# Performance work log

Hardware: AMD Instinct MI355X
Metric: run time of the kernel (lower is better)

## Reference

```python
import jax, jax.numpy as jnp
import numpy as np
import math


def _favor(X, W, is_query):
    # X: [B,L,H,M], W: [M,M] (shared across batch, matching tf.repeat of a single QR matrix)
    M = X.shape[-1]
    dn = 1.0 / math.sqrt(math.sqrt(M))
    X = dn * X
    diag = (jnp.sum(X * X, axis=-1) * (0.5 * dn * dn))[..., None]  # [B,L,H,1]
    dot = jnp.einsum('dm,blhm->blhd', W, X)                         # [B,L,H,M]
    if is_query:
        mx = jnp.max(X, axis=-1, keepdims=True)
    else:
        mx = jnp.max(X, axis=(1, 3), keepdims=True)  # axes (-3,-1) = (L, M)
    return (1.0 / math.sqrt(M)) * jnp.exp(dot - diag - mx + 1e-8)


def _causal_attn(qs, ks, vs):
    # qs,ks: [B,L,H,M]; vs: [B,L,H,D]. Cumulative KV-state recurrence via lax.scan.
    B, L, H, M = ks.shape
    D = vs.shape[-1]

    def step(carry, x):
        sums, snorm = carry          # [B,H,M,D], [B,H,M]
        q, k, v = x                  # [B,H,M], [B,H,M], [B,H,D]
        snorm = snorm + k
        sums = sums + k[..., :, None] * v[..., None, :]
        num = jnp.einsum('bhmd,bhm->bhd', sums, q)
        den = jnp.sum(q * snorm, axis=-1, keepdims=True)
        return (sums, snorm), num / den

    init = (jnp.zeros((B, H, M, D), qs.dtype), jnp.zeros((B, H, M), qs.dtype))
    xs = (jnp.swapaxes(qs, 0, 1), jnp.swapaxes(ks, 0, 1), jnp.swapaxes(vs, 0, 1))
    _, out = jax.lax.scan(step, init, xs)   # out: [L,B,H,D]
    return jnp.swapaxes(out, 0, 1)          # [B,L,H,D]


def _make_favor_proj(rng, M):
    # Mirrors: W ~ N(0,1); Q,_ = qr(W); Q /= norm(Q, axis=-1) (TF broadcast divides columns); Q *= sqrt(M)
    W = rng.standard_normal((M, M)).astype(np.float32)
    Q, _ = np.linalg.qr(W)
    n = np.linalg.norm(Q, axis=1)          # row norms, shape (M,)
    Q = Q / n[None, :]                     # TF broadcasting quirk: divide column j by n[j]
    return jnp.asarray(Q * math.sqrt(M), dtype=jnp.float32)


def setup_inputs() -> dict:
    B, L, d_model, H = 2, 4096, 1024, 16
    M = d_model // H
    key = jax.random.key(0)
    k1, k2, k3 = jax.random.split(key, 3)
    rng = np.random.default_rng(0)

    def dense_w(dout):
        return jnp.asarray(rng.standard_normal((d_model, dout)).astype(np.float32) * 0.02)

    return {
        'queries': jax.random.normal(k1, (B, L, d_model), jnp.float32),
        'keys': jax.random.normal(k2, (B, L, d_model), jnp.float32),
        'values': jax.random.normal(k3, (B, L, d_model), jnp.float32),
        'Wq': dense_w(H * M), 'bq': jnp.zeros((H * M,), jnp.float32),
        'Wk': dense_w(H * M), 'bk': jnp.zeros((H * M,), jnp.float32),
        'Wv': dense_w(H * M), 'bv': jnp.zeros((H * M,), jnp.float32),
        'Wo': dense_w(d_model), 'bo': jnp.zeros((d_model,), jnp.float32),
        'Wfq': _make_favor_proj(rng, M),
        'Wfk': _make_favor_proj(rng, M),
        'H': H,
    }


def reference(queries, keys, values, Wq, bq, Wk, bk, Wv, bv, Wo, bo, Wfq, Wfk, H):
    N, L, _ = queries.shape
    S = keys.shape[1]
    q = (queries @ Wq + bq).reshape(N, L, H, -1)
    k = (keys @ Wk + bk).reshape(N, S, H, -1)
    v = (values @ Wv + bv).reshape(N, S, H, -1)
    Ql = _favor(q, Wfq, is_query=True)
    Kl = _favor(k, Wfk, is_query=False)
    V = _causal_attn(Ql, Kl, v)             # [N,L,H,D]
    return V.reshape(N, L, -1) @ Wo + bo    # [N,L,d_model]
```

## Files before the change

### kernel.cpp

```cpp
#include <hip/hip_runtime.h>
#include <math.h>

#define BATCH 2
#define SEQ   4096
#define DM    1024
#define NH    16
#define MD    64
#define NROW  (BATCH*SEQ)
#define RQ    (BATCH*SEQ*NH)
#define NCHUNK 64
#define CT     64
#define DN    0.35355339059327373f
#define INV_SQRT_M 0.125f
#define PITCH 72
#define STSZ  (65*64)
#define DIAG_SCALE (0.125f * 0.0625f)

typedef unsigned short ushort_t;
typedef short bf8_t __attribute__((ext_vector_type(8)));
typedef float f4_t  __attribute__((ext_vector_type(4)));
typedef ushort_t us8_t __attribute__((ext_vector_type(8)));

__device__ static inline ushort_t f2bf(float f) {
    union { float f; unsigned u; } v; v.f = f;
    unsigned r = v.u + 0x7FFFu + ((v.u >> 16) & 1u);
    return (ushort_t)(r >> 16);
}
__device__ static inline float bf2f(ushort_t u) {
    union { unsigned u; float f; } v; v.u = ((unsigned)u) << 16;
    return v.f;
}

__device__ static inline void async_ld16(const ushort_t* g, ushort_t* l) {
    __builtin_amdgcn_global_load_lds(
        (const __attribute__((address_space(1))) unsigned int*)g,
        (__attribute__((address_space(3))) unsigned int*)l,
        16, 0, 0);
}

__device__ static inline void sbar() {
    __builtin_amdgcn_sched_barrier(0);
    __builtin_amdgcn_s_barrier();
    __builtin_amdgcn_sched_barrier(0);
}
#define VMCNT(n) do { asm volatile("s_waitcnt vmcnt(" #n ")" ::: "memory"); \
                      __builtin_amdgcn_sched_barrier(0); } while (0)

__device__ static inline void swz256(int bx, int* bm, int* bn) {
    const int xcd = bx & 7, s = bx >> 3;
    *bm = (xcd * 8 + (s >> 2)) << 7;
    *bn = (s & 3) << 8;
}

#define ABUF (128*64)
#define BBUF (256*64)

__device__ static inline void gemm128_core(
    const ushort_t* __restrict__ A, const ushort_t* __restrict__ BT,
    ushort_t* As, ushort_t* Bs, int bm, int bn, int tid, f4_t acc[4][4])
{
    const int lane = tid & 63, w = tid >> 6;
    const int wr = w >> 2, wc = w & 3;
    const int quad = lane >> 4, l15 = lane & 15;
    const int lrow = lane >> 3;
    const int kcol = ((lane & 7) ^ lrow) * 8;

    auto stB = [&](int t, int s) {
        #pragma unroll
        for (int c = 0; c < 4; ++c) {
            const int r0 = c * 64 + w * 8;
            async_ld16(BT + (size_t)(bn + r0 + lrow) * DM + t * 64 + kcol,
                       &Bs[s * BBUF + r0 * 64]);
        }
    };
    auto stA1 = [&](int t, int s) {
        const int r0 = (w < 4) ? w * 8 : 32 + w * 8;
        async_ld16(A + (size_t)(bm + r0 + lrow) * DM + t * 64 + kcol,
                   &As[s * ABUF + r0 * 64]);
    };
    auto stA2 = [&](int t, int s) {
        const int r0 = (w < 4) ? 32 + w * 8 : 64 + w * 8;
        async_ld16(A + (size_t)(bm + r0 + lrow) * DM + t * 64 + kcol,
                   &As[s * ABUF + r0 * 64]);
    };

    auto loadB = [&](int s, bf8_t bf[2][4]) {
        #pragma unroll
        for (int ks = 0; ks < 2; ++ks) {
            const int slot8 = (((ks << 2) | quad) ^ (l15 & 7)) * 8;
            #pragma unroll
            for (int j = 0; j < 4; ++j) {
                const int row = wc * 64 + j * 16 + l15;
                bf[ks][j] = *(const bf8_t*)&Bs[s * BBUF + row * 64 + slot8];
            }
        }
    };
    auto loadA = [&](int s, int ih, bf8_t af[2][2]) {
        #pragma unroll
        for (int ks = 0; ks < 2; ++ks) {
            const int slot8 = (((ks << 2) | quad) ^ (l15 & 7)) * 8;
            #pragma unroll
            for (int i = 0; i < 2; ++i) {
                const int row = wr * 64 + (ih * 2 + i) * 16 + l15;
                af[ks][i] = *(const bf8_t*)&As[s * ABUF + row * 64 + slot8];
            }
        }
    };
    auto mfma16 = [&](int ih, bf8_t af[2][2], bf8_t bf[2][4]) {
        __builtin_amdgcn_s_setprio(1);
        #pragma unroll
        for (int ks = 0; ks < 2; ++ks)
            #pragma unroll
            for (int i = 0; i < 2; ++i)
                #pragma unroll
                for (int j = 0; j < 4; ++j)
                    acc[ih * 2 + i][j] = __builtin_amdgcn_mfma_f32_16x16x32_bf16(
                        af[ks][i], bf[ks][j], acc[ih * 2 + i][j], 0, 0, 0);
        __builtin_amdgcn_s_setprio(0);
    };

    stB(0, 0); stA1(0, 0);
    stA2(0, 0);
    stB(1, 1); stA1(1, 1);
    VMCNT(6);
    sbar();

    bf8_t bf[2][4], af[2][2];
    #pragma unroll 1
    for (int v = 0; v < 7; ++v) {
        const int u0 = 2 * v;
        loadB(0, bf); loadA(0, 0, af);
        stA2(u0 + 1, 1);
        VMCNT(6); sbar();
        mfma16(0, af, bf);
        sbar();
        loadA(0, 1, af);
        stB(u0 + 2, 0); stA1(u0 + 2, 0);
        VMCNT(6); sbar();
        mfma16(1, af, bf);
        sbar();
        loadB(1, bf); loadA(1, 0, af);
        stA2(u0 + 2, 0);
        VMCNT(6); sbar();
        mfma16(0, af, bf);
        sbar();
        loadA(1, 1, af);
        stB(u0 + 3, 1); stA1(u0 + 3, 1);
        VMCNT(6); sbar();
        mfma16(1, af, bf);
        sbar();
    }
    loadB(0, bf); loadA(0, 0, af);
    stA2(15, 1);
    VMCNT(6); sbar();
    mfma16(0, af, bf);
    sbar();
    loadA(0, 1, af);
    VMCNT(1); sbar();
    mfma16(1, af, bf);
    sbar();
    loadB(1, bf); loadA(1, 0, af);
    VMCNT(0); sbar();
    mfma16(0, af, bf);
    sbar();
    loadA(1, 1, af);
    mfma16(1, af, bf);
}

__global__ __launch_bounds__(256) void prep_weights(
    const float* __restrict__ W0, const float* __restrict__ W1,
    const float* __restrict__ W2, const float* __restrict__ W3,
    ushort_t* __restrict__ WT, unsigned* __restrict__ kmOrd)
{
    if (blockIdx.z == 0 && blockIdx.x == 0 && blockIdx.y == 0 && threadIdx.x < 32)
        kmOrd[threadIdx.x] = 0u;
    const float* W = blockIdx.z == 0 ? W0 : (blockIdx.z == 1 ? W1 : (blockIdx.z == 2 ? W2 : W3));
    ushort_t* dst = WT + (size_t)blockIdx.z * DM * DM;
    __shared__ float t[32][33];
    const int k0 = blockIdx.x * 32, n0 = blockIdx.y * 32;
    const int tx = threadIdx.x & 31, ty = threadIdx.x >> 5;
    #pragma unroll
    for (int r = 0; r < 32; r += 8)
        t[ty + r][tx] = W[(size_t)(k0 + ty + r) * 1024 + n0 + tx];
    __syncthreads();
    #pragma unroll
    for (int r = 0; r < 32; r += 8)
        dst[(size_t)(n0 + ty + r) * 1024 + k0 + tx] = f2bf(t[tx][ty + r]);
}

__global__ __launch_bounds__(256) void cvt_qkv(
    const float* __restrict__ Q, const float* __restrict__ K,
    const float* __restrict__ V, ushort_t* __restrict__ Y)
{
    const int y = blockIdx.y;
    const float* X = y == 0 ? Q : (y == 1 ? K : V);
    ushort_t* dst = Y + (size_t)y * NROW * DM;
    int i = blockIdx.x * 256 + threadIdx.x;
    const float4* X4 = (const float4*)X;
    float4 a = X4[i * 2], b = X4[i * 2 + 1];
    us8_t o;
    o[0]=f2bf(a.x); o[1]=f2bf(a.y); o[2]=f2bf(a.z); o[3]=f2bf(a.w);
    o[4]=f2bf(b.x); o[5]=f2bf(b.y); o[6]=f2bf(b.z); o[7]=f2bf(b.w);
    *(us8_t*)&dst[i * 8] = o;
}

__global__ __launch_bounds__(512, 2) void gemm_qkv(
    const ushort_t* __restrict__ Xc, const ushort_t* __restrict__ WT,
    const float* __restrict__ bq, const float* __restrict__ bk,
    const float* __restrict__ bv, ushort_t* __restrict__ Obase,
    unsigned* __restrict__ kmOrd)
{
    __shared__ ushort_t As[2 * ABUF];
    __shared__ ushort_t Bs[2 * BBUF];
    const int z = blockIdx.y;
    const ushort_t* A  = Xc + (size_t)z * NROW * DM;
    const ushort_t* BT = WT + (size_t)z * DM * DM;
    const float* bias = z == 0 ? bq : (z == 1 ? bk : bv);
    ushort_t* Cbf = Obase + (size_t)z * NROW * DM;

    const int tid = threadIdx.x;
    int bm, bn;
    swz256(blockIdx.x, &bm, &bn);
    const int lane = tid & 63, w = tid >> 6;
    const int wr = w >> 2, wc = w & 3;
    const int quad = lane >> 4, l15 = lane & 15;

    f4_t acc[4][4] = {};
    gemm128_core(A, BT, As, Bs, bm, bn, tid, acc);

    float mx = -3.4e38f;
    #pragma unroll
    for (int j = 0; j < 4; ++j) {
        const int col = bn + wc * 64 + j * 16 + l15;
        const float bb = bias[col];
        #pragma unroll
        for (int i = 0; i < 4; ++i) {
            const int row0 = bm + wr * 64 + i * 16 + quad * 4;
            #pragma unroll
            for (int r = 0; r < 4; ++r) {
                float v = acc[i][j][r] + bb;
                mx = fmaxf(mx, v);
                Cbf[(size_t)(row0 + r) * DM + col] = f2bf(v);
            }
        }
    }
    if (z == 1) {
        #pragma unroll
        for (int off = 32; off; off >>= 1) mx = fmaxf(mx, __shfl_xor(mx, off));
        if (lane == 0) {
            const int b = bm >> 12;
            const int h = (bn + wc * 64) >> 6;
            unsigned ub = __float_as_uint(mx);
            unsigned enc = (ub & 0x80000000u) ? ~ub : (ub | 0x80000000u);
            atomicMax(&kmOrd[b * NH + h], enc);
        }
    }
}

__global__ __launch_bounds__(512, 2) void gemm_out(
    const ushort_t* __restrict__ A, const ushort_t* __restrict__ BT,
    const float* __restrict__ bias, float* __restrict__ C)
{
    __shared__ ushort_t As[2 * ABUF];
    __shared__ ushort_t Bs[2 * BBUF];
    const int tid = threadIdx.x;
    int bm, bn;
    swz256(blockIdx.x, &bm, &bn);
    const int lane = tid & 63, w = tid >> 6;
    const int wr = w >> 2, wc = w & 3;
    const int quad = lane >> 4, l15 = lane & 15;

    f4_t acc[4][4] = {};
    gemm128_core(A, BT, As, Bs, bm, bn, tid, acc);

    #pragma unroll
    for (int j = 0; j < 4; ++j) {
        const int col = bn + wc * 64 + j * 16 + l15;
        const float bb = bias[col];
        #pragma unroll
        for (int i = 0; i < 4; ++i) {
            const int row0 = bm + wr * 64 + i * 16 + quad * 4;
            #pragma unroll
            for (int r = 0; r < 4; ++r)
                C[(size_t)(row0 + r) * DM + col] = acc[i][j][r] + bb;
        }
    }
}

__global__ __launch_bounds__(256) void chunk_sums_mfma(
    const ushort_t* __restrict__ Kbf, const ushort_t* __restrict__ Vbf,
    const float* __restrict__ Wfk, const unsigned* __restrict__ kmOrd,
    ushort_t* __restrict__ ST)
{
    const int bx = blockIdx.x;
    const int c = bx & 63, h = (bx >> 6) & 15, b = bx >> 10;
    __shared__ ushort_t Ks[64 * PITCH];
    __shared__ ushort_t Kt[64 * PITCH];
    __shared__ ushort_t Vt[80 * PITCH];
    __shared__ ushort_t Ws[64 * PITCH];
    __shared__ float ssp[64][4];
    __shared__ float diag[64];
    const int tid = threadIdx.x;
    const int lane = tid & 63, w = tid >> 6;
    const int quad = lane >> 4, l15 = lane & 15;

    const size_t gbase = ((size_t)(b * SEQ + c * CT)) * DM + h * MD;

    #pragma unroll
    for (int r = 0; r < 2; ++r) {
        int idx = tid + r * 256;
        int row = idx >> 3, ch = idx & 7;
        *(us8_t*)&Ks[row * PITCH + ch * 8] =
            *(const us8_t*)&Kbf[gbase + (size_t)row * DM + ch * 8];
    }
    #pragma unroll
    for (int r = 0; r < 2; ++r) {
        int ch = w + r * 4;
        int t = lane;
        us8_t vv = *(const us8_t*)&Vbf[gbase + (size_t)t * DM + ch * 8];
        #pragma unroll
        for (int j = 0; j < 8; ++j) Vt[(ch * 8 + j) * PITCH + t] = vv[j];
    }
    if (tid < 64) Vt[64 * PITCH + tid] = (ushort_t)0x3F80;
    const float4* Wf4 = (const float4*)Wfk;
    #pragma unroll
    for (int i = 0; i < 4; ++i) {
        int f4i = tid + i * 256;
        int row = f4i >> 4, q4 = f4i & 15;
        float4 wv = Wf4[f4i];
        Ws[row * PITCH + q4 * 4 + 0] = f2bf(DN * wv.x);
        Ws[row * PITCH + q4 * 4 + 1] = f2bf(DN * wv.y);
        Ws[row * PITCH + q4 * 4 + 2] = f2bf(DN * wv.z);
        Ws[row * PITCH + q4 * 4 + 3] = f2bf(DN * wv.w);
    }
    __syncthreads();

    {
        const int row = tid >> 2, seg = tid & 3;
        const us8_t* xp = (const us8_t*)&Ks[row * PITCH + seg * 16];
        us8_t a = xp[0], b2 = xp[1];
        float ss = 0.f;
        #pragma unroll
        for (int j = 0; j < 8; ++j) {
            float x0 = bf2f(a[j]), x1 = bf2f(b2[j]);
            ss += x0 * x0 + x1 * x1;
        }
        ssp[row][seg] = ss;
    }
    __syncthreads();
    if (tid < 64)
        diag[tid] = (ssp[tid][0] + ssp[tid][1] + ssp[tid][2] + ssp[tid][3]) * DIAG_SCALE;
    unsigned u = kmOrd[b * NH + h];
    unsigned bits = (u & 0x80000000u) ? (u & 0x7FFFFFFFu) : ~u;
    const float mxs = DN * __uint_as_float(bits);
    __syncthreads();

    {
        bf8_t xf[2];
        #pragma unroll
        for (int ks = 0; ks < 2; ++ks)
            xf[ks] = *(const bf8_t*)&Ks[(w * 16 + l15) * PITCH + ks * 32 + quad * 8];
        f4_t facc[4] = {};
        #pragma unroll
        for (int dt = 0; dt < 4; ++dt)
            #pragma unroll
            for (int ks = 0; ks < 2; ++ks) {
                bf8_t wfr = *(const bf8_t*)&Ws[(dt * 16 + l15) * PITCH + ks * 32 + quad * 8];
                facc[dt] = __builtin_amdgcn_mfma_f32_16x16x32_bf16(xf[ks], wfr, facc[dt], 0, 0, 0);
            }
        #pragma unroll
        for (int r = 0; r < 4; ++r) {
            int t = w * 16 + quad * 4 + r;
            float d_ = diag[t];
            #pragma unroll
            for (int dt = 0; dt < 4; ++dt) {
                float e = facc[dt][r] - d_ - mxs + 1e-8f;
                Kt[(dt * 16 + l15) * PITCH + t] = f2bf(INV_SQRT_M * expf(e));
            }
        }
    }
    __syncthreads();

    ushort_t* Sg = ST + (size_t)((b * NH + h) * NCHUNK + c) * STSZ;

    bf8_t vf[2];
    #pragma unroll
    for (int ks = 0; ks < 2; ++ks)
        vf[ks] = *(const bf8_t*)&Vt[(w * 16 + l15) * PITCH + ks * 32 + quad * 8];
    f4_t acc[4] = {};
    #pragma unroll
    for (int mt = 0; mt < 4; ++mt)
        #pragma unroll
        for (int ks = 0; ks < 2; ++ks) {
            bf8_t kf = *(const bf8_t*)&Kt[(mt * 16 + l15) * PITCH + ks * 32 + quad * 8];
            acc[mt] = __builtin_amdgcn_mfma_f32_16x16x32_bf16(vf[ks], kf, acc[mt], 0, 0, 0);
        }
    #pragma unroll
    for (int mt = 0; mt < 4; ++mt)
        #pragma unroll
        for (int r = 0; r < 4; ++r)
            Sg[(w * 16 + quad * 4 + r) * 64 + mt * 16 + l15] = f2bf(acc[mt][r]);

    if (w == 0) {
        bf8_t vf4[2];
        #pragma unroll
        for (int ks = 0; ks < 2; ++ks)
            vf4[ks] = *(const bf8_t*)&Vt[(64 + l15) * PITCH + ks * 32 + quad * 8];
        f4_t accz[4] = {};
        #pragma unroll
        for (int mt = 0; mt < 4; ++mt)
            #pragma unroll
            for (int ks = 0; ks < 2; ++ks) {
                bf8_t kf = *(const bf8_t*)&Kt[(mt * 16 + l15) * PITCH + ks * 32 + quad * 8];
                accz[mt] = __builtin_amdgcn_mfma_f32_16x16x32_bf16(vf4[ks], kf, accz[mt], 0, 0, 0);
            }
        if (quad == 0) {
            #pragma unroll
            for (int mt = 0; mt < 4; ++mt)
                Sg[64 * 64 + mt * 16 + l15] = f2bf(accz[mt][0]);
        }
    }
}

__global__ __launch_bounds__(256) void prefix_scan_st(ushort_t* __restrict__ ST)
{
    const int sb = blockIdx.x / 17;
    const int e = (blockIdx.x % 17) * 256 + threadIdx.x;
    if (e >= STSZ) return;
    ushort_t* p = ST + (size_t)sb * NCHUNK * STSZ + e;
    ushort_t v[NCHUNK];
    #pragma unroll
    for (int c = 0; c < NCHUNK; ++c) v[c] = p[(size_t)c * STSZ];
    float run = 0.f;
    #pragma unroll
    for (int c = 0; c < NCHUNK; ++c) {
        float cur = bf2f(v[c]);
        p[(size_t)c * STSZ] = f2bf(run);
        run += cur;
    }
}

__global__ __launch_bounds__(256) void intra_attn_mfma(
    const ushort_t* __restrict__ Qraw, const ushort_t* __restrict__ Kbf,
    const ushort_t* __restrict__ Vbf, const ushort_t* __restrict__ ST,
    const float* __restrict__ Wfq, const float* __restrict__ Wfk,
    const unsigned* __restrict__ kmOrd, ushort_t* __restrict__ Obf)
{
    const int bx = blockIdx.x;
    const int c = bx & 63, h = (bx >> 6) & 15, b = bx >> 10;
    __shared__ ushort_t Qs[64 * PITCH];
    __shared__ ushort_t Ks[64 * PITCH];
    __shared__ ushort_t Vt[80 * PITCH];
    __shared__ ushort_t St[80 * PITCH];
    __shared__ ushort_t Ws[64 * PITCH];
    __shared__ float ssp[64][4];
    __shared__ float mxp[64][4];
    __shared__ float diag[64], mxr[64], dens[64];
    const int tid = threadIdx.x;
    const int lane = tid & 63, w = tid >> 6;
    const int quad = lane >> 4, l15 = lane & 15;

    const size_t gbase = ((size_t)(b * SEQ + c * CT)) * DM + h * MD;

    #pragma unroll
    for (int r = 0; r < 2; ++r) {
        int idx = tid + r * 256;
        int row = idx >> 3, ch = idx & 7;
        us8_t qv = *(const us8_t*)&Qraw[gbase + (size_t)row * DM + ch * 8];
        us8_t kv = *(const us8_t*)&Kbf[gbase + (size_t)row * DM + ch * 8];
        *(us8_t*)&Qs[row * PITCH + ch * 8] = qv;
        *(us8_t*)&Ks[row * PITCH + ch * 8] = kv;
    }
    #pragma unroll
    for (int r = 0; r < 2; ++r) {
        int ch = w + r * 4;
        int t = lane;
        us8_t vv = *(const us8_t*)&Vbf[gbase + (size_t)t * DM + ch * 8];
        #pragma unroll
        for (int j = 0; j < 8; ++j) Vt[(ch * 8 + j) * PITCH + t] = vv[j];
    }
    #pragma unroll
    for (int r = 0; r < 4; ++r) {
        int idx = tid + r * 256;
        int row = 64 + (idx >> 6), t = idx & 63;
        Vt[row * PITCH + t] = (row == 64) ? (ushort_t)0x3F80 : (ushort_t)0;
    }
    const us8_t* Sg8 = (const us8_t*)(ST + (size_t)((b * NH + h) * NCHUNK + c) * STSZ);
    #pragma unroll
    for (int r = 0; r < 3; ++r) {
        int idx = tid + r * 256;
        if (idx < 520) {
            int d = idx >> 3, mo = (idx & 7) * 8;
            *(us8_t*)&St[d * PITCH + mo] = Sg8[idx];
        }
        int idx2 = idx - 520;
        if (idx2 >= 0 && idx2 < 120) {
            int row = 65 + (idx2 >> 3), mo = (idx2 & 7) * 8;
            us8_t z = {};
            *(us8_t*)&St[row * PITCH + mo] = z;
        }
    }
    const float4* Wq4 = (const float4*)Wfq;
    #pragma unroll
    for (int i = 0; i < 4; ++i) {
        int f4i = tid + i * 256;
        int row = f4i >> 4, q4 = f4i & 15;
        float4 wv = Wq4[f4i];
        Ws[row * PITCH + q4 * 4 + 0] = f2bf(DN * wv.x);
        Ws[row * PITCH + q4 * 4 + 1] = f2bf(DN * wv.y);
        Ws[row * PITCH + q4 * 4 + 2] = f2bf(DN * wv.z);
        Ws[row * PITCH + q4 * 4 + 3] = f2bf(DN * wv.w);
    }
    __syncthreads();

    {
        const int row = tid >> 2, seg = tid & 3;
        const us8_t* xp = (const us8_t*)&Qs[row * PITCH + seg * 16];
        us8_t a = xp[0], b2 = xp[1];
        float ss = 0.f, mx = -3.4e38f;
        #pragma unroll
        for (int j = 0; j < 8; ++j) {
            float x0 = bf2f(a[j]), x1 = bf2f(b2[j]);
            ss += x0 * x0 + x1 * x1;
            mx = fmaxf(mx, fmaxf(x0, x1));
        }
        ssp[row][seg] = ss;
        mxp[row][seg] = mx;
    }
    __syncthreads();
    if (tid < 64) {
        diag[tid] = (ssp[tid][0] + ssp[tid][1] + ssp[tid][2] + ssp[tid][3]) * DIAG_SCALE;
        mxr[tid] = DN * fmaxf(fmaxf(mxp[tid][0], mxp[tid][1]),
                              fmaxf(mxp[tid][2], mxp[tid][3]));
    }
    __syncthreads();

    {
        bf8_t xf[2];
        #pragma unroll
        for (int ks = 0; ks < 2; ++ks)
            xf[ks] = *(const bf8_t*)&Qs[(w * 16 + l15) * PITCH + ks * 32 + quad * 8];
        f4_t facc[4] = {};
        #pragma unroll
        for (int dt = 0; dt < 4; ++dt)
            #pragma unroll
            for (int ks = 0; ks < 2; ++ks) {
                bf8_t wfr = *(const bf8_t*)&Ws[(dt * 16 + l15) * PITCH + ks * 32 + quad * 8];
                facc[dt] = __builtin_amdgcn_mfma_f32_16x16x32_bf16(xf[ks], wfr, facc[dt], 0, 0, 0);
            }
        __syncthreads();
        #pragma unroll
        for (int r = 0; r < 4; ++r) {
            int row = w * 16 + quad * 4 + r;
            float d_ = diag[row], m_ = mxr[row];
            #pragma unroll
            for (int dt = 0; dt < 4; ++dt) {
                float e = facc[dt][r] - d_ - m_ + 1e-8f;
                Qs[row * PITCH + dt * 16 + l15] = f2bf(INV_SQRT_M * expf(e));
            }
        }
    }
    __syncthreads();

    const float4* Wk4 = (const float4*)Wfk;
    #pragma unroll
    for (int i = 0; i < 4; ++i) {
        int f4i = tid + i * 256;
        int row = f4i >> 4, q4 = f4i & 15;
        float4 wv = Wk4[f4i];
        Ws[row * PITCH + q4 * 4 + 0] = f2bf(DN * wv.x);
        Ws[row * PITCH + q4 * 4 + 1] = f2bf(DN * wv.y);
        Ws[row * PITCH + q4 * 4 + 2] = f2bf(DN * wv.z);
        Ws[row * PITCH + q4 * 4 + 3] = f2bf(DN * wv.w);
    }
    {
        const int row = tid >> 2, seg = tid & 3;
        const us8_t* xp = (const us8_t*)&Ks[row * PITCH + seg * 16];
        us8_t a = xp[0], b2 = xp[1];
        float ss = 0.f;
        #pragma unroll
        for (int j = 0; j < 8; ++j) {
            float x0 = bf2f(a[j]), x1 = bf2f(b2[j]);
            ss += x0 * x0 + x1 * x1;
        }
        ssp[row][seg] = ss;
    }
    __syncthreads();
    if (tid < 64)
        diag[tid] = (ssp[tid][0] + ssp[tid][1] + ssp[tid][2] + ssp[tid][3]) * DIAG_SCALE;
    unsigned ku = kmOrd[b * NH + h];
    unsigned kbits = (ku & 0x80000000u) ? (ku & 0x7FFFFFFFu) : ~ku;
    const float mxs = DN * __uint_as_float(kbits);
    __syncthreads();

    {
        bf8_t xf[2];
        #pragma unroll
        for (int ks = 0; ks < 2; ++ks)
            xf[ks] = *(const bf8_t*)&Ks[(w * 16 + l15) * PITCH + ks * 32 + quad * 8];
        f4_t facc[4] = {};
        #pragma unroll
        for (int dt = 0; dt < 4; ++dt)
            #pragma unroll
            for (int ks = 0; ks < 2; ++ks) {
                bf8_t wfr = *(const bf8_t*)&Ws[(dt * 16 + l15) * PITCH + ks * 32 + quad * 8];
                facc[dt] = __builtin_amdgcn_mfma_f32_16x16x32_bf16(xf[ks], wfr, facc[dt], 0, 0, 0);
            }
        __syncthreads();
        #pragma unroll
        for (int r = 0; r < 4; ++r) {
            int row = w * 16 + quad * 4 + r;
            float d_ = diag[row];
            #pragma unroll
            for (int dt = 0; dt < 4; ++dt) {
                float e = facc[dt][r] - d_ - mxs + 1e-8f;
                Ks[row * PITCH + dt * 16 + l15] = f2bf(INV_SQRT_M * expf(e));
            }
        }
    }
    __syncthreads();

    bf8_t qf[2];
    #pragma unroll
    for (int ks = 0; ks < 2; ++ks)
        qf[ks] = *(const bf8_t*)&Qs[(w * 16 + l15) * PITCH + ks * 32 + quad * 8];
    f4_t accA[4] = {};
    #pragma unroll
    for (int jt = 0; jt < 4; ++jt)
        #pragma unroll
        for (int ks = 0; ks < 2; ++ks) {
            bf8_t kf = *(const bf8_t*)&Ks[(jt * 16 + l15) * PITCH + ks * 32 + quad * 8];
            accA[jt] = __builtin_amdgcn_mfma_f32_16x16x32_bf16(qf[ks], kf, accA[jt], 0, 0, 0);
        }
    __syncthreads();
    #pragma unroll
    for (int jt = 0; jt < 4; ++jt) {
        int j = jt * 16 + l15;
        #pragma unroll
        for (int r = 0; r < 4; ++r) {
            int i = w * 16 + quad * 4 + r;
            float a = (j <= i) ? accA[jt][r] : 0.f;
            Ks[i * PITCH + j] = f2bf(a);
        }
    }
    __syncthreads();

    bf8_t af[2];
    #pragma unroll
    for (int ks = 0; ks < 2; ++ks)
        af[ks] = *(const bf8_t*)&Ks[(w * 16 + l15) * PITCH + ks * 32 + quad * 8];
    f4_t acc[5] = {};
    #pragma unroll
    for (int dt = 0; dt < 5; ++dt)
        #pragma unroll
        for (int ks = 0; ks < 2; ++ks) {
            bf8_t sf = *(const bf8_t*)&St[(dt * 16 + l15) * PITCH + ks * 32 + quad * 8];
            acc[dt] = __builtin_amdgcn_mfma_f32_16x16x32_bf16(qf[ks], sf, acc[dt], 0, 0, 0);
            bf8_t vf = *(const bf8_t*)&Vt[(dt * 16 + l15) * PITCH + ks * 32 + quad * 8];
            acc[dt] = __builtin_amdgcn_mfma_f32_16x16x32_bf16(af[ks], vf, acc[dt], 0, 0, 0);
        }
    if (l15 == 0) {
        #pragma unroll
        for (int r = 0; r < 4; ++r) dens[w * 16 + quad * 4 + r] = acc[4][r];
    }
    __syncthreads();

    #pragma unroll
    for (int r = 0; r < 4; ++r) {
        int i = w * 16 + quad * 4 + r;
        float inv = 1.0f / dens[i];
        #pragma unroll
        for (int dt = 0; dt < 4; ++dt)
            Obf[gbase + (size_t)i * DM + dt * 16 + l15] = f2bf(acc[dt][r] * inv);
    }
}

extern "C" void kernel_launch(void* const* d_in, const int* in_sizes, int n_in,
                              void* d_out, int out_size, void* d_ws, size_t ws_size,
                              hipStream_t stream)
{
    const float* queries = (const float*)d_in[0];
    const float* keys    = (const float*)d_in[1];
    const float* values  = (const float*)d_in[2];
    const float* Wq = (const float*)d_in[3];  const float* bq = (const float*)d_in[4];
    const float* Wk = (const float*)d_in[5];  const float* bk = (const float*)d_in[6];
    const float* Wv = (const float*)d_in[7];  const float* bv = (const float*)d_in[8];
    const float* Wo = (const float*)d_in[9];  const float* bo = (const float*)d_in[10];
    const float* Wfq = (const float*)d_in[11];
    const float* Wfk = (const float*)d_in[12];

    char* ws = (char*)d_ws;
    unsigned* kmOrd = (unsigned*)ws;
    ushort_t* STb = (ushort_t*)(ws + 256);
    ushort_t* qbf = STb + (size_t)32 * NCHUNK * STSZ;
    ushort_t* kbf = qbf + (size_t)NROW * DM;
    ushort_t* vbf = kbf + (size_t)NROW * DM;
    ushort_t* obf = vbf + (size_t)NROW * DM;
    ushort_t* xcvt = obf + (size_t)NROW * DM;
    ushort_t* wT  = xcvt + (size_t)3 * NROW * DM;
    ushort_t* WoT = wT + (size_t)3 * DM * DM;

    prep_weights<<<dim3(32, 32, 4), 256, 0, stream>>>(Wq, Wk, Wv, Wo, wT, kmOrd);

    const int n8 = NROW * DM / 8;
    cvt_qkv<<<dim3(n8 / 256, 3), 256, 0, stream>>>(queries, keys, values, xcvt);

    gemm_qkv<<<dim3(256, 3), 512, 0, stream>>>(xcvt, wT, bq, bk, bv, qbf, kmOrd);

    chunk_sums_mfma<<<BATCH * NH * NCHUNK, 256, 0, stream>>>(kbf, vbf, Wfk, kmOrd, STb);
    prefix_scan_st<<<32 * 17, 256, 0, stream>>>(STb);
    intra_attn_mfma<<<BATCH * NH * NCHUNK, 256, 0, stream>>>(qbf, kbf, vbf, STb,
                                                             Wfq, Wfk, kmOrd, obf);

    gemm_out<<<256, 512, 0, stream>>>(obf, WoT, bo, (float*)d_out);
}
```

Before: 313.3 us.

## Replace 128x256 GEMM tiles with 128x128 tiles and simpler double-buffered pipeline

Both projection GEMMs move from 512-thread blocks with 128x256 output tiles and a finely interleaved split-A pipeline to 256-thread blocks with 128x128 tiles and a plain two-stage double buffer. The launch grid doubles (512 blocks per GEMM), and the XCD swizzle is updated to match. The aim is more blocks, better spread across CUs, and a simpler schedule with less LDS per block. The cost is lower arithmetic intensity per tile, since B is reused across only 128 columns, and less fine-grained overlap of loads with MFMAs.

```diff
diff --git a/kernel.cpp b/kernel.cpp
--- a/kernel.cpp
+++ b/kernel.cpp
@@ -46,125 +46,82 @@
 #define VMCNT(n) do { asm volatile("s_waitcnt vmcnt(" #n ")" ::: "memory"); \
                       __builtin_amdgcn_sched_barrier(0); } while (0)
 
-__device__ static inline void swz256(int bx, int* bm, int* bn) {
-    const int xcd = bx & 7, s = bx >> 3;
-    *bm = (xcd * 8 + (s >> 2)) << 7;
-    *bn = (s & 3) << 8;
-}
-
-#define ABUF (128*64)
-#define BBUF (256*64)
-
-__device__ static inline void gemm128_core(
+#define TBUF (128*64)
+
+__device__ static inline void gemm_tile_core(
     const ushort_t* __restrict__ A, const ushort_t* __restrict__ BT,
     ushort_t* As, ushort_t* Bs, int bm, int bn, int tid, f4_t acc[4][4])
 {
     const int lane = tid & 63, w = tid >> 6;
-    const int wr = w >> 2, wc = w & 3;
+    const int wr = w >> 1, wc = w & 1;
     const int quad = lane >> 4, l15 = lane & 15;
     const int lrow = lane >> 3;
     const int kcol = ((lane & 7) ^ lrow) * 8;
 
+    auto stA = [&](int t, int s) {
+        #pragma unroll
+        for (int c = 0; c < 4; ++c) {
+            const int r0 = c * 32 + w * 8;
+            async_ld16(A + (size_t)(bm + r0 + lrow) * DM + t * 64 + kcol,
+                       &As[s * TBUF + r0 * 64]);
+        }
+    };
     auto stB = [&](int t, int s) {
         #pragma unroll
         for (int c = 0; c < 4; ++c) {
-            const int r0 = c * 64 + w * 8;
+            const int r0 = c * 32 + w * 8;
             async_ld16(BT + (size_t)(bn + r0 + lrow) * DM + t * 64 + kcol,
-                       &Bs[s * BBUF + r0 * 64]);
+                       &Bs[s * TBUF + r0 * 64]);
         }
     };
-    auto stA1 = [&](int t, int s) {
-        const int r0 = (w < 4) ? w * 8 : 32 + w * 8;
-        async_ld16(A + (size_t)(bm + r0 + lrow) * DM + t * 64 + kcol,
-                   &As[s * ABUF + r0 * 64]);
+
+    bf8_t af[4], bf[4];
+    auto rdFrags = [&](int s, int ks) {
+        const int slot8 = (((ks << 2) | quad) ^ (l15 & 7)) * 8;
+        #pragma unroll
+        for (int i = 0; i < 4; ++i)
+            af[i] = *(const bf8_t*)&As[s * TBUF + (wr * 64 + i * 16 + l15) * 64 + slot8];
+        #pragma unroll
+        for (int j = 0; j < 4; ++j)
+            bf[j] = *(const bf8_t*)&Bs[s * TBUF + (wc * 64 + j * 16 + l15) * 64 + slot8];
     };
-    auto stA2 = [&](int t, int s) {
-        const int r0 = (w < 4) ? 32 + w * 8 : 64 + w * 8;
-        async_ld16(A + (size_t)(bm + r0 + lrow) * DM + t * 64 + kcol,
-                   &As[s * ABUF + r0 * 64]);
-    };
-
-    auto loadB = [&](int s, bf8_t bf[2][4]) {
-        #pragma unroll
-        for (int ks = 0; ks < 2; ++ks) {
-            const int slot8 = (((ks << 2) | quad) ^ (l15 & 7)) * 8;
-            #pragma unroll
-            for (int j = 0; j < 4; ++j) {
-                const int row = wc * 64 + j * 16 + l15;
-                bf[ks][j] = *(const bf8_t*)&Bs[s * BBUF + row * 64 + slot8];
-            }
-        }
-    };
-    auto loadA = [&](int s, int ih, bf8_t af[2][2]) {
-        #pragma unroll
-        for (int ks = 0; ks < 2; ++ks) {
-            const int slot8 = (((ks << 2) | quad) ^ (l15 & 7)) * 8;
-            #pragma unroll
-            for (int i = 0; i < 2; ++i) {
-                const int row = wr * 64 + (ih * 2 + i) * 16 + l15;
-                af[ks][i] = *(const bf8_t*)&As[s * ABUF + row * 64 + slot8];
-            }
-        }
-    };
-    auto mfma16 = [&](int ih, bf8_t af[2][2], bf8_t bf[2][4]) {
+    auto mm = [&]() {
         __builtin_amdgcn_s_setprio(1);
         #pragma unroll
-        for (int ks = 0; ks < 2; ++ks)
-            #pragma unroll
-            for (int i = 0; i < 2; ++i)
-                #pragma unroll
-                for (int j = 0; j < 4; ++j)
-                    acc[ih * 2 + i][j] = __builtin_amdgcn_mfma_f32_16x16x32_bf16(
-                        af[ks][i], bf[ks][j], acc[ih * 2 + i][j], 0, 0, 0);
+        for (int i = 0; i < 4; ++i)
+            #pragma unroll
+            for (int j = 0; j < 4; ++j)
+                acc[i][j] = __builtin_amdgcn_mfma_f32_16x16x32_bf16(
+                    af[i], bf[j], acc[i][j], 0, 0, 0);
         __builtin_amdgcn_s_setprio(0);
     };
 
-    stB(0, 0); stA1(0, 0);
-    stA2(0, 0);
-    stB(1, 1); stA1(1, 1);
-    VMCNT(6);
+    stA(0, 0); stB(0, 0);
+
+    #pragma unroll 1
+    for (int t = 0; t < 15; ++t) {
+        const int s = t & 1;
+        stA(t + 1, s ^ 1); stB(t + 1, s ^ 1);
+        VMCNT(8);
+        sbar();
+        rdFrags(s, 0);
+        mm();
+        rdFrags(s, 1);
+        mm();
+        sbar();
+    }
+    VMCNT(0);
     sbar();
-
-    bf8_t bf[2][4], af[2][2];
-    #pragma unroll 1
-    for (int v = 0; v < 7; ++v) {
-        const int u0 = 2 * v;
-        loadB(0, bf); loadA(0, 0, af);
-        stA2(u0 + 1, 1);
-        VMCNT(6); sbar();
-        mfma16(0, af, bf);
-        sbar();
-        loadA(0, 1, af);
-        stB(u0 + 2, 0); stA1(u0 + 2, 0);
-        VMCNT(6); sbar();
-        mfma16(1, af, bf);
-        sbar();
-        loadB(1, bf); loadA(1, 0, af);
-        stA2(u0 + 2, 0);
-        VMCNT(6); sbar();
-        mfma16(0, af, bf);
-        sbar();
-        loadA(1, 1, af);
-        stB(u0 + 3, 1); stA1(u0 + 3, 1);
-        VMCNT(6); sbar();
-        mfma16(1, af, bf);
-        sbar();
-    }
-    loadB(0, bf); loadA(0, 0, af);
-    stA2(15, 1);
-    VMCNT(6); sbar();
-    mfma16(0, af, bf);
-    sbar();
-    loadA(0, 1, af);
-    VMCNT(1); sbar();
-    mfma16(1, af, bf);
-    sbar();
-    loadB(1, bf); loadA(1, 0, af);
-    VMCNT(0); sbar();
-    mfma16(0, af, bf);
-    sbar();
-    loadA(1, 1, af);
-    mfma16(1, af, bf);
+    rdFrags(1, 0);
+    mm();
+    rdFrags(1, 1);
+    mm();
+}
+
+__device__ static inline void swz512(int bx, int* bm, int* bn) {
+    const int xcd = bx & 7, s = bx >> 3;
+    *bm = (xcd * 8 + (s >> 3)) << 7;
+    *bn = (s & 7) << 7;
 }
 
 __global__ __launch_bounds__(256) void prep_weights(
@@ -204,14 +161,14 @@
     *(us8_t*)&dst[i * 8] = o;
 }
 
-__global__ __launch_bounds__(512, 2) void gemm_qkv(
+__global__ __launch_bounds__(256, 2) void gemm_qkv(
     const ushort_t* __restrict__ Xc, const ushort_t* __restrict__ WT,
     const float* __restrict__ bq, const float* __restrict__ bk,
     const float* __restrict__ bv, ushort_t* __restrict__ Obase,
     unsigned* __restrict__ kmOrd)
 {
-    __shared__ ushort_t As[2 * ABUF];
-    __shared__ ushort_t Bs[2 * BBUF];
+    __shared__ ushort_t As[2 * TBUF];
+    __shared__ ushort_t Bs[2 * TBUF];
     const int z = blockIdx.y;
     const ushort_t* A  = Xc + (size_t)z * NROW * DM;
     const ushort_t* BT = WT + (size_t)z * DM * DM;
@@ -220,13 +177,13 @@
 
     const int tid = threadIdx.x;
     int bm, bn;
-    swz256(blockIdx.x, &bm, &bn);
+    swz512(blockIdx.x, &bm, &bn);
     const int lane = tid & 63, w = tid >> 6;
-    const int wr = w >> 2, wc = w & 3;
+    const int wr = w >> 1, wc = w & 1;
     const int quad = lane >> 4, l15 = lane & 15;
 
     f4_t acc[4][4] = {};
-    gemm128_core(A, BT, As, Bs, bm, bn, tid, acc);
+    gemm_tile_core(A, BT, As, Bs, bm, bn, tid, acc);
 
     float mx = -3.4e38f;
     #pragma unroll
@@ -257,21 +214,21 @@
     }
 }
 
-__global__ __launch_bounds__(512, 2) void gemm_out(
+__global__ __launch_bounds__(256, 2) void gemm_out(
     const ushort_t* __restrict__ A, const ushort_t* __restrict__ BT,
     const float* __restrict__ bias, float* __restrict__ C)
 {
-    __shared__ ushort_t As[2 * ABUF];
-    __shared__ ushort_t Bs[2 * BBUF];
+    __shared__ ushort_t As[2 * TBUF];
+    __shared__ ushort_t Bs[2 * TBUF];
     const int tid = threadIdx.x;
     int bm, bn;
-    swz256(blockIdx.x, &bm, &bn);
+    swz512(blockIdx.x, &bm, &bn);
     const int lane = tid & 63, w = tid >> 6;
-    const int wr = w >> 2, wc = w & 3;
+    const int wr = w >> 1, wc = w & 1;
     const int quad = lane >> 4, l15 = lane & 15;
 
     f4_t acc[4][4] = {};
-    gemm128_core(A, BT, As, Bs, bm, bn, tid, acc);
+    gemm_tile_core(A, BT, As, Bs, bm, bn, tid, acc);
 
     #pragma unroll
     for (int j = 0; j < 4; ++j) {
@@ -705,12 +662,12 @@
     const int n8 = NROW * DM / 8;
     cvt_qkv<<<dim3(n8 / 256, 3), 256, 0, stream>>>(queries, keys, values, xcvt);
 
-    gemm_qkv<<<dim3(256, 3), 512, 0, stream>>>(xcvt, wT, bq, bk, bv, qbf, kmOrd);
+    gemm_qkv<<<dim3(512, 3), 256, 0, stream>>>(xcvt, wT, bq, bk, bv, qbf, kmOrd);
 
     chunk_sums_mfma<<<BATCH * NH * NCHUNK, 256, 0, stream>>>(kbf, vbf, Wfk, kmOrd, STb);
     prefix_scan_st<<<32 * 17, 256, 0, stream>>>(STb);
     intra_attn_mfma<<<BATCH * NH * NCHUNK, 256, 0, stream>>>(qbf, kbf, vbf, STb,
                                                              Wfq, Wfk, kmOrd, obf);
 
-    gemm_out<<<256, 512, 0, stream>>>(obf, WoT, bo, (float*)d_out);
-}
+    gemm_out<<<512, 256, 0, stream>>>(obf, WoT, bo, (float*)d_out);
+}
```

New measurement: 310.7 us. About the same (-0.8%).

## Use 128x128 tiles for output GEMM and merge weight prep with input conversion

Applied to the files above, without the earlier changes.

The output projection GEMM moves from 128x256 tiles with 512 threads to 128x128 tiles with 256 threads and 512 blocks. It uses a new double-buffered core loop and a matching XCD swizzle, so more blocks fill the 256 CUs and the LDS footprint drops. Separately, the weight transpose/convert kernel and the QKV fp32-to-bf16 conversion kernel are merged into one launch to save a kernel launch and its tail. The smaller tiles lower per-block data reuse and add redundant A/B loads.

```diff
diff --git a/kernel.cpp b/kernel.cpp
--- a/kernel.cpp
+++ b/kernel.cpp
@@ -46,14 +46,9 @@
 #define VMCNT(n) do { asm volatile("s_waitcnt vmcnt(" #n ")" ::: "memory"); \
                       __builtin_amdgcn_sched_barrier(0); } while (0)
 
-__device__ static inline void swz256(int bx, int* bm, int* bn) {
-    const int xcd = bx & 7, s = bx >> 3;
-    *bm = (xcd * 8 + (s >> 2)) << 7;
-    *bn = (s & 3) << 8;
-}
-
 #define ABUF (128*64)
 #define BBUF (256*64)
+#define TBUF (128*64)
 
 __device__ static inline void gemm128_core(
     const ushort_t* __restrict__ A, const ushort_t* __restrict__ BT,
@@ -167,17 +162,118 @@
     mfma16(1, af, bf);
 }
 
-__global__ __launch_bounds__(256) void prep_weights(
+__device__ static inline void swz256(int bx, int* bm, int* bn) {
+    const int xcd = bx & 7, s = bx >> 3;
+    *bm = (xcd * 8 + (s >> 2)) << 7;
+    *bn = (s & 3) << 8;
+}
+
+__device__ static inline void gemm_tile_core(
+    const ushort_t* __restrict__ A, const ushort_t* __restrict__ BT,
+    ushort_t* As, ushort_t* Bs, int bm, int bn, int tid, f4_t acc[4][4])
+{
+    const int lane = tid & 63, w = tid >> 6;
+    const int wr = w >> 1, wc = w & 1;
+    const int quad = lane >> 4, l15 = lane & 15;
+    const int lrow = lane >> 3;
+    const int kcol = ((lane & 7) ^ lrow) * 8;
+
+    auto stA = [&](int t, int s) {
+        #pragma unroll
+        for (int c = 0; c < 4; ++c) {
+            const int r0 = c * 32 + w * 8;
+            async_ld16(A + (size_t)(bm + r0 + lrow) * DM + t * 64 + kcol,
+                       &As[s * TBUF + r0 * 64]);
+        }
+    };
+    auto stB = [&](int t, int s) {
+        #pragma unroll
+        for (int c = 0; c < 4; ++c) {
+            const int r0 = c * 32 + w * 8;
+            async_ld16(BT + (size_t)(bn + r0 + lrow) * DM + t * 64 + kcol,
+                       &Bs[s * TBUF + r0 * 64]);
+        }
+    };
+
+    bf8_t af[4], bf[4];
+    auto rdFrags = [&](int s, int ks) {
+        const int slot8 = (((ks << 2) | quad) ^ (l15 & 7)) * 8;
+        #pragma unroll
+        for (int i = 0; i < 4; ++i)
+            af[i] = *(const bf8_t*)&As[s * TBUF + (wr * 64 + i * 16 + l15) * 64 + slot8];
+        #pragma unroll
+        for (int j = 0; j < 4; ++j)
+            bf[j] = *(const bf8_t*)&Bs[s * TBUF + (wc * 64 + j * 16 + l15) * 64 + slot8];
+    };
+    auto mm = [&]() {
+        __builtin_amdgcn_s_setprio(1);
+        #pragma unroll
+        for (int i = 0; i < 4; ++i)
+            #pragma unroll
+            for (int j = 0; j < 4; ++j)
+                acc[i][j] = __builtin_amdgcn_mfma_f32_16x16x32_bf16(
+                    af[i], bf[j], acc[i][j], 0, 0, 0);
+        __builtin_amdgcn_s_setprio(0);
+    };
+
+    stA(0, 0); stB(0, 0);
+
+    #pragma unroll 1
+    for (int t = 0; t < 15; ++t) {
+        const int s = t & 1;
+        stA(t + 1, s ^ 1); stB(t + 1, s ^ 1);
+        VMCNT(8);
+        sbar();
+        rdFrags(s, 0);
+        mm();
+        rdFrags(s, 1);
+        mm();
+        sbar();
+    }
+    VMCNT(0);
+    sbar();
+    rdFrags(1, 0);
+    mm();
+    rdFrags(1, 1);
+    mm();
+}
+
+__device__ static inline void swz512(int bx, int* bm, int* bn) {
+    const int xcd = bx & 7, s = bx >> 3;
+    *bm = (xcd * 8 + (s >> 3)) << 7;
+    *bn = (s & 7) << 7;
+}
+
+__global__ __launch_bounds__(256) void prep_cvt(
+    const float* __restrict__ Q, const float* __restrict__ K,
+    const float* __restrict__ V, ushort_t* __restrict__ Y,
     const float* __restrict__ W0, const float* __restrict__ W1,
     const float* __restrict__ W2, const float* __restrict__ W3,
     ushort_t* __restrict__ WT, unsigned* __restrict__ kmOrd)
 {
-    if (blockIdx.z == 0 && blockIdx.x == 0 && blockIdx.y == 0 && threadIdx.x < 32)
-        kmOrd[threadIdx.x] = 0u;
-    const float* W = blockIdx.z == 0 ? W0 : (blockIdx.z == 1 ? W1 : (blockIdx.z == 2 ? W2 : W3));
-    ushort_t* dst = WT + (size_t)blockIdx.z * DM * DM;
+    const int bx = blockIdx.x;
+    if (bx < 12288) {
+        const int y = bx >> 12;
+        const float* X = y == 0 ? Q : (y == 1 ? K : V);
+        ushort_t* dst = Y + (size_t)y * NROW * DM;
+        int i = (bx & 4095) * 256 + threadIdx.x;
+        const float4* X4 = (const float4*)X;
+        float4 a = X4[i * 2], b = X4[i * 2 + 1];
+        us8_t o;
+        o[0]=f2bf(a.x); o[1]=f2bf(a.y); o[2]=f2bf(a.z); o[3]=f2bf(a.w);
+        o[4]=f2bf(b.x); o[5]=f2bf(b.y); o[6]=f2bf(b.z); o[7]=f2bf(b.w);
+        *(us8_t*)&dst[i * 8] = o;
+        return;
+    }
+    const int pbx = bx - 12288;
+    if (pbx == 0 && threadIdx.x < 32) kmOrd[threadIdx.x] = 0u;
+    const int z = pbx >> 10;
+    const int rem = pbx & 1023;
+    const int kx = rem & 31, ny = rem >> 5;
+    const float* W = z == 0 ? W0 : (z == 1 ? W1 : (z == 2 ? W2 : W3));
+    ushort_t* dst = WT + (size_t)z * DM * DM;
     __shared__ float t[32][33];
-    const int k0 = blockIdx.x * 32, n0 = blockIdx.y * 32;
+    const int k0 = kx * 32, n0 = ny * 32;
     const int tx = threadIdx.x & 31, ty = threadIdx.x >> 5;
     #pragma unroll
     for (int r = 0; r < 32; r += 8)
@@ -186,22 +282,6 @@
     #pragma unroll
     for (int r = 0; r < 32; r += 8)
         dst[(size_t)(n0 + ty + r) * 1024 + k0 + tx] = f2bf(t[tx][ty + r]);
-}
-
-__global__ __launch_bounds__(256) void cvt_qkv(
-    const float* __restrict__ Q, const float* __restrict__ K,
-    const float* __restrict__ V, ushort_t* __restrict__ Y)
-{
-    const int y = blockIdx.y;
-    const float* X = y == 0 ? Q : (y == 1 ? K : V);
-    ushort_t* dst = Y + (size_t)y * NROW * DM;
-    int i = blockIdx.x * 256 + threadIdx.x;
-    const float4* X4 = (const float4*)X;
-    float4 a = X4[i * 2], b = X4[i * 2 + 1];
-    us8_t o;
-    o[0]=f2bf(a.x); o[1]=f2bf(a.y); o[2]=f2bf(a.z); o[3]=f2bf(a.w);
-    o[4]=f2bf(b.x); o[5]=f2bf(b.y); o[6]=f2bf(b.z); o[7]=f2bf(b.w);
-    *(us8_t*)&dst[i * 8] = o;
 }
 
 __global__ __launch_bounds__(512, 2) void gemm_qkv(
@@ -257,21 +337,21 @@
     }
 }
 
-__global__ __launch_bounds__(512, 2) void gemm_out(
+__global__ __launch_bounds__(256, 2) void gemm_out(
     const ushort_t* __restrict__ A, const ushort_t* __restrict__ BT,
     const float* __restrict__ bias, float* __restrict__ C)
 {
-    __shared__ ushort_t As[2 * ABUF];
-    __shared__ ushort_t Bs[2 * BBUF];
+    __shared__ ushort_t As[2 * TBUF];
+    __shared__ ushort_t Bs[2 * TBUF];
     const int tid = threadIdx.x;
     int bm, bn;
-    swz256(blockIdx.x, &bm, &bn);
+    swz512(blockIdx.x, &bm, &bn);
     const int lane = tid & 63, w = tid >> 6;
-    const int wr = w >> 2, wc = w & 3;
+    const int wr = w >> 1, wc = w & 1;
     const int quad = lane >> 4, l15 = lane & 15;
 
     f4_t acc[4][4] = {};
-    gemm128_core(A, BT, As, Bs, bm, bn, tid, acc);
+    gemm_tile_core(A, BT, As, Bs, bm, bn, tid, acc);
 
     #pragma unroll
     for (int j = 0; j < 4; ++j) {
@@ -700,10 +780,8 @@
     ushort_t* wT  = xcvt + (size_t)3 * NROW * DM;
     ushort_t* WoT = wT + (size_t)3 * DM * DM;
 
-    prep_weights<<<dim3(32, 32, 4), 256, 0, stream>>>(Wq, Wk, Wv, Wo, wT, kmOrd);
-
-    const int n8 = NROW * DM / 8;
-    cvt_qkv<<<dim3(n8 / 256, 3), 256, 0, stream>>>(queries, keys, values, xcvt);
+    prep_cvt<<<16384, 256, 0, stream>>>(queries, keys, values, xcvt,
+                                        Wq, Wk, Wv, Wo, wT, kmOrd);
 
     gemm_qkv<<<dim3(256, 3), 512, 0, stream>>>(xcvt, wT, bq, bk, bv, qbf, kmOrd);
 
@@ -712,5 +790,5 @@
     intra_attn_mfma<<<BATCH * NH * NCHUNK, 256, 0, stream>>>(qbf, kbf, vbf, STb,
                                                              Wfq, Wfk, kmOrd, obf);
 
-    gemm_out<<<256, 512, 0, stream>>>(obf, WoT, bo, (float*)d_out);
-}
+    gemm_out<<<512, 256, 0, stream>>>(obf, WoT, bo, (float*)d_out);
+}
```

New measurement: 308.1 us. Within noise of the previous version (-1.7%).
